# Performance work log

Measured on AMD Instinct MI355X. Metric: run time of the kernel, lower is better.

The kernel has to match this reference:

```python
import jax, jax.numpy as jnp
import numpy as np
from jax import lax

P = 8; E = 192; D_MODEL = E + 4; D_STATE = 16; D_CONV = 4; EXPAND = 2
D_INNER = EXPAND * D_MODEL  # 392
DT_RANK = -(-D_MODEL // 16)  # 13
MAX_FREQ = 32


def silu(v):
    return v * jax.nn.sigmoid(v)


def layernorm(v, g, b, eps=1e-5):
    m = v.mean(-1, keepdims=True)
    var = v.var(-1, keepdims=True)
    return (v - m) / jnp.sqrt(var + eps) * g + b


def mamba(x, in_w, conv_w, conv_b, xp_w, dt_w, dt_b, A_log, Dp, out_w):
    # Standard mamba_ssm Mamba block. x: (B, L, d_model)
    B, L, _ = x.shape
    xz = x @ in_w.T                      # (B,L,2*d_inner)
    xi, z = jnp.split(xz, 2, axis=-1)
    # depthwise causal conv1d (torch pads d_conv-1 both sides then truncates to L)
    xc = jnp.transpose(xi, (0, 2, 1))    # (B,d_inner,L)
    xc = lax.conv_general_dilated(xc, conv_w[:, None, :], (1,), [(D_CONV - 1, 0)],
                                  dimension_numbers=('NCH', 'OIH', 'NCH'),
                                  feature_group_count=D_INNER)
    xc = silu(jnp.transpose(xc, (0, 2, 1)) + conv_b)  # (B,L,d_inner)
    x_dbl = xc @ xp_w.T                  # (B,L,dt_rank+2*d_state)
    dt = x_dbl[..., :DT_RANK]
    Bm = x_dbl[..., DT_RANK:DT_RANK + D_STATE]
    Cm = x_dbl[..., DT_RANK + D_STATE:]
    delta = jax.nn.softplus(dt @ dt_w.T + dt_b)       # (B,L,d_inner)
    A = -jnp.exp(A_log)                               # (d_inner,d_state)
    deltaA = jnp.exp(delta[..., None] * A)            # (B,L,d_inner,d_state)
    deltaBu = delta[..., None] * Bm[:, :, None, :] * xc[..., None]

    def step(h, inp):
        dA, dBu, c = inp
        h = dA * h + dBu
        return h, jnp.einsum('bdn,bn->bd', h, c)

    h0 = jnp.zeros((B, D_INNER, D_STATE), x.dtype)
    _, ys = lax.scan(step, h0, (deltaA.transpose(1, 0, 2, 3),
                                deltaBu.transpose(1, 0, 2, 3),
                                Cm.transpose(1, 0, 2)))
    y = ys.transpose(1, 0, 2) + Dp * xc
    y = y * silu(z)
    return y @ out_w.T


def _mk_mamba_params(key):
    ks = jax.random.split(key, 6)
    s = 0.05
    return dict(
        in_w=jax.random.normal(ks[0], (2 * D_INNER, D_MODEL)) * s,
        conv_w=jax.random.normal(ks[1], (D_INNER, D_CONV)) * s,
        conv_b=jnp.zeros((D_INNER,)),
        xp_w=jax.random.normal(ks[2], (DT_RANK + 2 * D_STATE, D_INNER)) * s,
        dt_w=jax.random.normal(ks[3], (D_INNER, DT_RANK)) * s,
        dt_b=jax.random.normal(ks[4], (D_INNER,)) * 0.1,
        A_log=jnp.log(jnp.broadcast_to(jnp.arange(1, D_STATE + 1, dtype=jnp.float32), (D_INNER, D_STATE)) + 0.0),
        D=jnp.ones((D_INNER,)),
        out_w=jax.random.normal(ks[5], (D_MODEL, D_INNER)) * s,
    )


def setup_inputs() -> dict:
    key = jax.random.key(0)
    k = jax.random.split(key, 8)
    inp = {
        'x': jax.random.normal(k[0], (16, 3, 256, 256), dtype=jnp.float32),
        'patch_w': jax.random.normal(k[1], (E, 3, P, P)) * 0.05,
        'patch_b': jnp.zeros((E,)),
        'pe_ln_g': jnp.ones((E,)), 'pe_ln_b': jnp.zeros((E,)),
        'blk_ln_g': jnp.ones((D_MODEL,)), 'blk_ln_b': jnp.zeros((D_MODEL,)),
        'cls_w': jax.random.normal(k[2], (1, D_MODEL)) * 0.05,
        'cls_b': jnp.zeros((1,)),
    }
    for pref, kk in (('f_', k[3]), ('b_', k[4])):
        for name, val in _mk_mamba_params(kk).items():
            inp[pref + name] = val
    return inp


def reference(x, patch_w, patch_b, pe_ln_g, pe_ln_b,
              f_in_w, f_conv_w, f_conv_b, f_xp_w, f_dt_w, f_dt_b, f_A_log, f_D, f_out_w,
              b_in_w, b_conv_w, b_conv_b, b_xp_w, b_dt_w, b_dt_b, b_A_log, b_D, b_out_w,
              blk_ln_g, blk_ln_b, cls_w, cls_b):
    B, C, H, W = x.shape
    hp, wp = H // P, W // P
    # PatchEmbed: stride==kernel conv expressed as one GEMM over patches
    xp = x.reshape(B, C, hp, P, wp, P)
    tok = jnp.einsum('bchpwq,ecpq->bhwe', xp, patch_w) + patch_b
    tok = tok.reshape(B, hp * wp, E)
    tok = silu(layernorm(tok, pe_ln_g, pe_ln_b))
    # RotaryEmbedding: concat 4 positional channels
    L = hp * wp
    scale = 2 * np.pi / MAX_FREQ
    pos = jnp.arange(L, dtype=tok.dtype)[:, None] * scale
    row = (jnp.arange(L) // MAX_FREQ).astype(tok.dtype)[:, None] * scale
    cp = jnp.concatenate([jnp.sin(pos), jnp.cos(pos), jnp.sin(row), jnp.cos(row)], axis=-1)
    h = jnp.concatenate([tok, jnp.broadcast_to(cp[None], (B, L, 4))], axis=-1)  # (B,L,196)
    # BidirectionalMambaBlock
    fo = mamba(h, f_in_w, f_conv_w, f_conv_b, f_xp_w, f_dt_w, f_dt_b, f_A_log, f_D, f_out_w)
    bo = jnp.flip(mamba(jnp.flip(h, 1), b_in_w, b_conv_w, b_conv_b, b_xp_w, b_dt_w, b_dt_b, b_A_log, b_D, b_out_w), 1)
    out = (fo + bo) * 0.5
    out = silu(layernorm(out, blk_ln_g, blk_ln_b)) + h
    # Classifier: mean pool + linear (num_classes==2 -> 1 logit)
    return out.mean(1) @ cls_w.T + cls_b
```

## Files before the change

kernel.cpp:

```cpp
#include <hip/hip_runtime.h>
#include <cstdint>
#include <cstddef>

constexpr int B_   = 16;
constexpr int L_   = 1024;
constexpr int E_   = 192;
constexpr int DM   = 196;
constexpr int DI   = 392;
constexpr int DS   = 16;
constexpr int DTR  = 13;
constexpr int NTOK = B_ * L_;
constexpr int XDW  = DTR + 2 * DS;
constexpr int CH   = B_ * DI;

constexpr int KP_XZ = 224;
constexpr int KP_OP = 416;
constexpr int KP_PW = 192;

constexpr size_t HW_SZ = (size_t)NTOK * DM;
constexpr size_t DI_SZ = (size_t)NTOK * DI;

constexpr size_t O_H     = 0;
constexpr size_t O_H16   = 3211264;
constexpr size_t O_XI_F  = 5046272;
constexpr size_t O_XI_B  = 11468800;
constexpr size_t O_Z_F   = 17891328;
constexpr size_t O_Z_B   = 24313856;
constexpr size_t O_XC_F  = 30736384;
constexpr size_t O_XC_B  = 37158912;
constexpr size_t O_DTR_F = 43581440;
constexpr size_t O_DTR_B = 43794432;
constexpr size_t O_BC_F  = 44007424;
constexpr size_t O_BC_B  = 44531712;
constexpr size_t O_YS_F  = 45056000;
constexpr size_t O_YS_B  = 48267264;
constexpr size_t O_PW16  = 51478528;
constexpr size_t O_FIN16 = 51496960;
constexpr size_t O_BIN16 = 51584768;
constexpr size_t O_FOUT16= 51672576;
constexpr size_t O_BOUT16= 51713344;

typedef _Float16 half8 __attribute__((ext_vector_type(8)));
typedef _Float16 half4v __attribute__((ext_vector_type(4)));
typedef float f32x4v __attribute__((ext_vector_type(4)));

__device__ __forceinline__ float siluf(float x) {
    return x / (1.f + __expf(-x));
}
__device__ __forceinline__ float fexp2(float x) {
    return __builtin_amdgcn_exp2f(x);
}

__device__ __forceinline__ float blk_sum(float v, float* red) {
    #pragma unroll
    for (int o = 32; o > 0; o >>= 1) v += __shfl_down(v, o);
    int w = threadIdx.x >> 6;
    __syncthreads();
    if ((threadIdx.x & 63) == 0) red[w] = v;
    __syncthreads();
    return red[0] + red[1] + red[2] + red[3];
}

__global__ __launch_bounds__(256) void cvt_all(const float* __restrict__ pw,
                                               const float* __restrict__ fin,
                                               const float* __restrict__ bin,
                                               const float* __restrict__ fout,
                                               const float* __restrict__ bout,
                                               _Float16* __restrict__ dst) {
    int i = blockIdx.x * 256 + threadIdx.x;
    const float* src; int K, Kp, off;
    if (i < 36864)       { src = pw;   K = 192; Kp = 192; off = i; }
    else if (i < 212480) { src = fin;  K = 196; Kp = 224; off = i - 36864; }
    else if (i < 388096) { src = bin;  K = 196; Kp = 224; off = i - 212480; }
    else if (i < 469632) { src = fout; K = 392; Kp = 416; off = i - 388096; }
    else                 { src = bout; K = 392; Kp = 416; off = i - 469632; }
    int n = off / Kp, k = off - n * Kp;
    dst[i] = (_Float16)(k < K ? src[(size_t)n * K + k] : 0.f);
}

__global__ __launch_bounds__(256) void gather_patch(const float* __restrict__ x,
                                                    _Float16* __restrict__ Xp) {
    int i = blockIdx.x * 256 + threadIdx.x;
    int tok = i / 24, r = i - tok * 24;
    int c = r >> 3, p = r & 7;
    int b = tok >> 10, l = tok & 1023, hh = l >> 5, wv = l & 31;
    const float* src = x + (((size_t)(b * 3 + c) * 256 + hh * 8 + p) << 8) + wv * 8;
    float4 v0 = *(const float4*)src;
    float4 v1 = *(const float4*)(src + 4);
    half8 o;
    o[0] = (_Float16)v0.x; o[1] = (_Float16)v0.y; o[2] = (_Float16)v0.z; o[3] = (_Float16)v0.w;
    o[4] = (_Float16)v1.x; o[5] = (_Float16)v1.y; o[6] = (_Float16)v1.z; o[7] = (_Float16)v1.w;
    *(half8*)(Xp + (size_t)tok * 192 + c * 64 + p * 8) = o;
}

template <int MODE>
__device__ __forceinline__ void mfma_core(const _Float16* __restrict__ A,
                                          const _Float16* __restrict__ W,
                                          const float* __restrict__ bias,
                                          void* __restrict__ Cv_,
                                          int N, int Kpad, int ldc,
                                          int flip, int m_blk, int n_blk) {
    const int tid = threadIdx.x;
    const int wv = tid >> 6, lane = tid & 63;
    const int col = lane & 15, quad = lane >> 4;
    const int m_base = m_blk * 128 + wv * 32;
    const int n_base = n_blk * 64;

    int r0 = m_base + col, r1 = m_base + 16 + col;
    if (flip) {
        r0 = (r0 & ~1023) + (1023 - (r0 & 1023));
        r1 = (r1 & ~1023) + (1023 - (r1 & 1023));
    }
    const _Float16* a0p = A + (size_t)r0 * Kpad + quad * 8;
    const _Float16* a1p = A + (size_t)r1 * Kpad + quad * 8;

    const _Float16* bp[4];
    bool bok[4];
    #pragma unroll
    for (int j = 0; j < 4; ++j) {
        int n = n_base + j * 16 + col;
        bok[j] = (n < N);
        bp[j] = W + (size_t)(bok[j] ? n : 0) * Kpad + quad * 8;
    }

    f32x4v acc[2][4];
    #pragma unroll
    for (int i = 0; i < 2; ++i)
        #pragma unroll
        for (int j = 0; j < 4; ++j)
            #pragma unroll
            for (int r = 0; r < 4; ++r) acc[i][j][r] = 0.f;

    half8 bzero;
    #pragma unroll
    for (int q = 0; q < 8; ++q) bzero[q] = (_Float16)0.f;

    for (int k0 = 0; k0 < Kpad; k0 += 32) {
        half8 a0 = *(const half8*)(a0p + k0);
        half8 a1 = *(const half8*)(a1p + k0);
        #pragma unroll
        for (int j = 0; j < 4; ++j) {
            half8 bv = bzero;
            if (bok[j]) bv = *(const half8*)(bp[j] + k0);
            acc[0][j] = __builtin_amdgcn_mfma_f32_16x16x32_f16(a0, bv, acc[0][j], 0, 0, 0);
            acc[1][j] = __builtin_amdgcn_mfma_f32_16x16x32_f16(a1, bv, acc[1][j], 0, 0, 0);
        }
    }

    if constexpr (MODE == 0) {
        float* C = (float*)Cv_;
        #pragma unroll
        for (int i = 0; i < 2; ++i) {
            int mrow = m_base + i * 16 + quad * 4;
            #pragma unroll
            for (int j = 0; j < 4; ++j) {
                int n = n_base + j * 16 + col;
                if (n < N) {
                    float bv = bias ? bias[n] : 0.f;
                    #pragma unroll
                    for (int r = 0; r < 4; ++r)
                        C[(size_t)(mrow + r) * ldc + n] = acc[i][j][r] + bv;
                }
            }
        }
    } else if constexpr (MODE == 2 || MODE == 3) {
        __shared__ _Float16 cst[64 * 136];
        #pragma unroll
        for (int i = 0; i < 2; ++i) {
            int t_loc = wv * 32 + i * 16 + quad * 4;
            #pragma unroll
            for (int j = 0; j < 4; ++j) {
                int n_loc = j * 16 + col;
                half4v v;
                #pragma unroll
                for (int r = 0; r < 4; ++r) {
                    float xx = acc[i][j][r];
                    if (MODE == 3) xx = xx / (1.f + __expf(-xx));
                    v[r] = (_Float16)xx;
                }
                *(half4v*)&cst[n_loc * 136 + t_loc] = v;
            }
        }
        __syncthreads();
        const int n_loc = tid >> 2, chunk = tid & 3;
        const int n = n_base + n_loc;
        if (n < N) {
            const int bb = (m_blk * 128) >> 10;
            const int t0b = (m_blk * 128) & 1023;
            _Float16* dst = (_Float16*)Cv_ + (((size_t)(bb * N + n)) << 10) + t0b + chunk * 32;
            const _Float16* s = &cst[n_loc * 136 + chunk * 32];
            #pragma unroll
            for (int q = 0; q < 4; ++q)
                *(half8*)(dst + q * 8) = *(const half8*)(s + q * 8);
        }
    } else {
        __shared__ _Float16 cst[128 * 72];
        #pragma unroll
        for (int i = 0; i < 2; ++i) {
            #pragma unroll
            for (int j = 0; j < 4; ++j) {
                int n_loc = j * 16 + col;
                #pragma unroll
                for (int r = 0; r < 4; ++r) {
                    int m_loc = wv * 32 + i * 16 + quad * 4 + r;
                    cst[m_loc * 72 + n_loc] = (_Float16)acc[i][j][r];
                }
            }
        }
        __syncthreads();
        const int m_loc = tid >> 1, half = tid & 1;
        const int m = m_blk * 128 + m_loc;
        _Float16* C = (_Float16*)Cv_;
        const _Float16* s = &cst[m_loc * 72 + half * 32];
        if (n_base + 64 <= N) {
            _Float16* dst = C + (size_t)m * ldc + n_base + half * 32;
            #pragma unroll
            for (int q = 0; q < 4; ++q)
                *(half8*)(dst + q * 8) = *(const half8*)(s + q * 8);
        } else {
            #pragma unroll
            for (int q = 0; q < 32; ++q) {
                int n = n_base + half * 32 + q;
                if (n < N) C[(size_t)m * ldc + n] = s[q];
            }
        }
    }
}

__global__ __launch_bounds__(256) void mfma_patch(const _Float16* __restrict__ A,
                                                  const _Float16* __restrict__ W,
                                                  const float* __restrict__ bias,
                                                  float* __restrict__ C) {
    mfma_core<0>(A, W, bias, C, 192, KP_PW, 192, 0, blockIdx.x, blockIdx.y);
}

__global__ __launch_bounds__(256) void mfma_xz(const _Float16* __restrict__ A,
                                               const _Float16* __restrict__ Wf,
                                               const _Float16* __restrict__ Wb,
                                               _Float16* __restrict__ C0, _Float16* __restrict__ C1,
                                               _Float16* __restrict__ C2, _Float16* __restrict__ C3) {
    const int zi = blockIdx.z;
    const _Float16* W = (zi < 2 ? Wf : Wb) + (size_t)(zi & 1) * DI * KP_XZ;
    const int flip = zi >> 1;
    if (zi == 0)      mfma_core<2>(A, W, nullptr, C0, DI, KP_XZ, 0, flip, blockIdx.x, blockIdx.y);
    else if (zi == 1) mfma_core<3>(A, W, nullptr, C1, DI, KP_XZ, 0, flip, blockIdx.x, blockIdx.y);
    else if (zi == 2) mfma_core<2>(A, W, nullptr, C2, DI, KP_XZ, 0, flip, blockIdx.x, blockIdx.y);
    else              mfma_core<3>(A, W, nullptr, C3, DI, KP_XZ, 0, flip, blockIdx.x, blockIdx.y);
}

__global__ __launch_bounds__(256) void mfma_op(const _Float16* __restrict__ Af,
                                               const _Float16* __restrict__ Ab,
                                               const _Float16* __restrict__ Wf,
                                               const _Float16* __restrict__ Wb,
                                               _Float16* __restrict__ Cf, _Float16* __restrict__ Cb) {
    const int zi = blockIdx.z;
    mfma_core<4>(zi ? Ab : Af, zi ? Wb : Wf, nullptr, zi ? Cb : Cf,
                 DM, KP_OP, DM, 0, blockIdx.x, blockIdx.y);
}

__global__ __launch_bounds__(256) void ln_silu_pos(const float* __restrict__ tok,
                                                   const float* __restrict__ g,
                                                   const float* __restrict__ bb,
                                                   _Float16* __restrict__ h16) {
    const int w = threadIdx.x >> 6, lane = threadIdx.x & 63;
    const int t = blockIdx.x * 4 + w;
    const float* tp = tok + (size_t)t * E_;
    float v[3];
    float s1 = 0.f, s2 = 0.f;
    #pragma unroll
    for (int i = 0; i < 3; ++i) {
        v[i] = tp[lane + i * 64];
        s1 += v[i];
        s2 = fmaf(v[i], v[i], s2);
    }
    #pragma unroll
    for (int o = 32; o > 0; o >>= 1) {
        s1 += __shfl_xor(s1, o);
        s2 += __shfl_xor(s2, o);
    }
    float mean = s1 * (1.f / E_);
    float var = s2 * (1.f / E_) - mean * mean;
    float inv = rsqrtf(var + 1e-5f);
    _Float16* hq = h16 + (size_t)t * KP_XZ;
    #pragma unroll
    for (int i = 0; i < 3; ++i) {
        int e = lane + i * 64;
        float o = siluf((v[i] - mean) * inv * g[e] + bb[e]);
        hq[e] = (_Float16)o;
    }
    const int l = t & 1023;
    const float scale = 0.19634954084936207f;
    if (lane < 4) {
        float pv = (lane == 0) ? sinf(l * scale)
                 : (lane == 1) ? cosf(l * scale)
                 : (lane == 2) ? sinf((float)(l >> 5) * scale)
                 :               cosf((float)(l >> 5) * scale);
        hq[E_ + lane] = (_Float16)pv;
    } else if (lane < 32) {
        hq[192 + lane] = (_Float16)0.f;
    }
}

__global__ __launch_bounds__(256) void gemm_xdbl(const _Float16* __restrict__ xi_f,
                                                 const _Float16* __restrict__ xi_b,
                                                 const float* __restrict__ Wf,
                                                 const float* __restrict__ Wb,
                                                 const float* __restrict__ fcw,
                                                 const float* __restrict__ fcb,
                                                 const float* __restrict__ bcw,
                                                 const float* __restrict__ bcb,
                                                 float* __restrict__ dtrf,
                                                 float* __restrict__ dtrb,
                                                 float* __restrict__ bcf,
                                                 float* __restrict__ bcb2,
                                                 _Float16* __restrict__ xcf,
                                                 _Float16* __restrict__ xcb) {
    const int yi = blockIdx.y;
    const _Float16* xi = yi ? xi_b : xi_f;
    const float* W = yi ? Wb : Wf;
    const float* cw = yi ? bcw : fcw;
    const float* cb = yi ? bcb : fcb;
    float* dtr = yi ? dtrb : dtrf;
    float* bc = yi ? bcb2 : bcf;
    _Float16* xc = yi ? xcb : xcf;
    __shared__ __align__(16) float As[16][68];
    __shared__ __align__(16) float Ws[16][68];
    const int m0 = blockIdx.x * 64;
    const int t = threadIdx.x;
    const int tx = t & 15, ty = t >> 4;
    float acc[4][4] = {};
    const int arow_l = t >> 2;
    const int kq = (t & 3) * 4;
    const int bb_ = m0 >> 10, tt0 = m0 & 1023;
    for (int kt = 0; kt < 25; ++kt) {
        const int k0 = kt << 4;
        {
            int kr = t >> 4, tc = t & 15;
            int kk = k0 + kr;
            float o4[4] = {0.f, 0.f, 0.f, 0.f};
            if (kk < DI) {
                const int tpos = tt0 + tc * 4;
                const _Float16* xp = xi + (((size_t)(bb_ * DI + kk)) << 10) + tpos;
                half4v cur = *(const half4v*)xp;
                half4v prv;
                if (tpos > 0) prv = *(const half4v*)(xp - 4);
                else { prv[0] = prv[1] = prv[2] = prv[3] = (_Float16)0.f; }
                float xw[7] = {(float)prv[1], (float)prv[2], (float)prv[3],
                               (float)cur[0], (float)cur[1], (float)cur[2], (float)cur[3]};
                float4 wv4 = *(const float4*)(cw + kk * 4);
                float wc[4] = {wv4.x, wv4.y, wv4.z, wv4.w};
                float bv = cb[kk];
                #pragma unroll
                for (int j = 0; j < 4; ++j) {
                    float a = bv;
                    #pragma unroll
                    for (int q = 0; q < 4; ++q) a = fmaf(xw[j + q], wc[q], a);
                    o4[j] = siluf(a);
                }
                half4v o4h;
                #pragma unroll
                for (int j = 0; j < 4; ++j) o4h[j] = (_Float16)o4[j];
                *(half4v*)(xc + (((size_t)(bb_ * DI + kk)) << 10) + tpos) = o4h;
            }
            *(float4*)&As[kr][tc * 4] = *(float4*)o4;
        }
        {
            bool okn = arow_l < XDW;
            const float* wp = W + (size_t)arow_l * DI;
            #pragma unroll
            for (int jj = 0; jj < 4; ++jj) {
                int kk = k0 + kq + jj;
                Ws[kq + jj][arow_l] = (okn && kk < DI) ? wp[kk] : 0.f;
            }
        }
        __syncthreads();
        #pragma unroll
        for (int k = 0; k < 16; ++k) {
            float av[4], wv[4];
            *(float4*)av = *(const float4*)&As[k][ty * 4];
            *(float4*)wv = *(const float4*)&Ws[k][tx * 4];
            #pragma unroll
            for (int i = 0; i < 4; ++i)
                #pragma unroll
                for (int j = 0; j < 4; ++j)
                    acc[i][j] = fmaf(av[i], wv[j], acc[i][j]);
        }
        __syncthreads();
    }
    #pragma unroll
    for (int i = 0; i < 4; ++i) {
        int m = m0 + ty * 4 + i;
        #pragma unroll
        for (int j = 0; j < 4; ++j) {
            int n = tx * 4 + j;
            float v = acc[i][j];
            if (n < DTR) dtr[(size_t)m * DTR + n] = v;
            else if (n < XDW) bc[(size_t)m * 32 + (n - DTR)] = v;
        }
    }
}

__global__ __launch_bounds__(256) void delta_kernel(
        const float* __restrict__ dtr_f, const float* __restrict__ dtr_b,
        _Float16* __restrict__ dlT_f, _Float16* __restrict__ dlT_b,
        const float* __restrict__ f_dt_w, const float* __restrict__ f_dt_b,
        const float* __restrict__ b_dt_w, const float* __restrict__ b_dt_b) {
    int i = blockIdx.x * 256 + threadIdx.x;
    int dir = i >= (int)DI_SZ;
    int j = dir ? i - (int)DI_SZ : i;
    int r = j >> 10, t = j & 1023;
    int b = r / DI, d = r - (r / DI) * DI;
    size_t tok = ((size_t)b << 10) + t;
    const float* xd = (dir ? dtr_b : dtr_f) + tok * DTR;
    const float* w = (dir ? b_dt_w : f_dt_w) + d * DTR;
    float acc = (dir ? b_dt_b : f_dt_b)[d];
    #pragma unroll
    for (int q = 0; q < DTR; ++q) acc = fmaf(xd[q], w[q], acc);
    float sp = fmaxf(acc, 0.f) + log1pf(__expf(-fabsf(acc)));
    (dir ? dlT_b : dlT_f)[j] = (_Float16)sp;
}

__global__ __launch_bounds__(256) __attribute__((amdgpu_waves_per_eu(4, 4)))
void scan_kernel(
        const _Float16* __restrict__ dlT_f, const _Float16* __restrict__ dlT_b,
        const _Float16* __restrict__ xcT_f, const _Float16* __restrict__ xcT_b,
        const float* __restrict__ bc_f,  const float* __restrict__ bc_b,
        const _Float16* __restrict__ zT_f, const _Float16* __restrict__ zT_b,
        _Float16* __restrict__ y16_f,    _Float16* __restrict__ y16_b,
        const float* __restrict__ fA, const float* __restrict__ bA,
        const float* __restrict__ fD, const float* __restrict__ bD) {
    __shared__ float sH[256][17];
    __shared__ float sPI[256][17];
    const int tid = threadIdx.x;
    const int ch_l = tid & 7;
    const int c    = tid >> 3;
    const int row  = tid;
    const int blk  = (blockIdx.x & 7) * 196 + (blockIdx.x >> 3);
    const int chain = blk * 8 + ch_l;
    const int dir = chain >= CH;
    const int r = chain - (dir ? CH : 0);
    const int b = r / DI, d = r - (r / DI) * DI;

    const _Float16* dlT = (dir ? dlT_b : dlT_f) + ((size_t)r << 10);
    const _Float16* uT  = (dir ? xcT_b : xcT_f) + ((size_t)r << 10);
    const _Float16* zT  = (dir ? zT_b : zT_f) + ((size_t)r << 10);
    const float* BC  = (dir ? bc_b  : bc_f)  + (((size_t)b << 10) * 32);
    _Float16* y16    = (dir ? y16_b : y16_f) + ((size_t)r << 10);
    const float* Al  = (dir ? bA : fA) + d * DS;
    float Av[16];
    #pragma unroll
    for (int i = 0; i < 16; ++i) Av[i] = -__expf(Al[i]) * 1.4426950408889634f;
    const float Dd = (dir ? bD : fD)[d];
    const int t0 = c << 5;

    if (c < 31) {
        float h[16];
        #pragma unroll
        for (int i = 0; i < 16; ++i) h[i] = 0.f;
        float S = 0.f;
        const float* bcp = BC + t0 * 32;
        const _Float16* dp = dlT + t0;
        const _Float16* up = uT + t0;
        for (int g = 0; g < 8; ++g) {
            half4v d4 = *(const half4v*)(dp + g * 4);
            half4v u4 = *(const half4v*)(up + g * 4);
            #pragma unroll
            for (int tt = 0; tt < 4; ++tt) {
                float dv = (float)d4[tt];
                float uv = (float)u4[tt];
                float w = dv * uv;
                S += dv;
                #pragma unroll
                for (int q = 0; q < 4; ++q) {
                    float4 Bq = *(const float4*)(bcp + tt * 32 + q * 4);
                    h[q*4+0] = fmaf(fexp2(dv * Av[q*4+0]), h[q*4+0], w * Bq.x);
                    h[q*4+1] = fmaf(fexp2(dv * Av[q*4+1]), h[q*4+1], w * Bq.y);
                    h[q*4+2] = fmaf(fexp2(dv * Av[q*4+2]), h[q*4+2], w * Bq.z);
                    h[q*4+3] = fmaf(fexp2(dv * Av[q*4+3]), h[q*4+3], w * Bq.w);
                }
            }
            bcp += 128;
        }
        #pragma unroll
        for (int i = 0; i < 16; ++i) {
            sPI[row][i] = fexp2(S * Av[i]);
            sH[row][i] = h[i];
        }
    }
    __syncthreads();

    if (tid < 128) {
        const int ch = tid >> 4, n = tid & 15;
        float hi = 0.f;
        #pragma unroll
        for (int cc = 0; cc < 32; ++cc) {
            const int rw = (cc << 3) | ch;
            float P = sPI[rw][n];
            float H = sH[rw][n];
            sPI[rw][n] = hi;
            if (cc < 31) hi = fmaf(P, hi, H);
        }
    }
    __syncthreads();

    {
        float h[16];
        #pragma unroll
        for (int i = 0; i < 16; ++i) h[i] = sPI[row][i];
        const float* bcp = BC + t0 * 32;
        const _Float16* dp = dlT + t0;
        const _Float16* up = uT + t0;
        const _Float16* zp = zT + t0;
        _Float16* yp = y16 + t0;
        for (int g8 = 0; g8 < 4; ++g8) {
            half8 zb = *(const half8*)(zp + g8 * 8);
            _Float16 ybuf[8] __attribute__((aligned(16)));
            #pragma unroll
            for (int gg = 0; gg < 2; ++gg) {
                half4v d4 = *(const half4v*)(dp + g8 * 8 + gg * 4);
                half4v u4 = *(const half4v*)(up + g8 * 8 + gg * 4);
                #pragma unroll
                for (int tt = 0; tt < 4; ++tt) {
                    float dv = (float)d4[tt];
                    float uv = (float)u4[tt];
                    float w = dv * uv;
                    float p = 0.f;
                    #pragma unroll
                    for (int q = 0; q < 4; ++q) {
                        float4 Bq = *(const float4*)(bcp + tt * 32 + q * 4);
                        float4 Cq = *(const float4*)(bcp + tt * 32 + 16 + q * 4);
                        h[q*4+0] = fmaf(fexp2(dv * Av[q*4+0]), h[q*4+0], w * Bq.x);
                        p = fmaf(h[q*4+0], Cq.x, p);
                        h[q*4+1] = fmaf(fexp2(dv * Av[q*4+1]), h[q*4+1], w * Bq.y);
                        p = fmaf(h[q*4+1], Cq.y, p);
                        h[q*4+2] = fmaf(fexp2(dv * Av[q*4+2]), h[q*4+2], w * Bq.z);
                        p = fmaf(h[q*4+2], Cq.z, p);
                        h[q*4+3] = fmaf(fexp2(dv * Av[q*4+3]), h[q*4+3], w * Bq.w);
                        p = fmaf(h[q*4+3], Cq.w, p);
                    }
                    ybuf[gg * 4 + tt] =
                        (_Float16)((p + Dd * uv) * (float)zb[gg * 4 + tt]);
                }
                bcp += 128;
            }
            *(half8*)(yp + g8 * 8) = *(half8*)ybuf;
        }
    }
}

__global__ __launch_bounds__(256) void transp_y(
        const _Float16* __restrict__ yf, const _Float16* __restrict__ yb,
        _Float16* __restrict__ of, _Float16* __restrict__ ob) {
    __shared__ _Float16 tile[64][72];
    const int dblk = blockIdx.z % 7, dir = blockIdx.z / 7;
    const int b = blockIdx.y, tb = blockIdx.x;
    const _Float16* y = dir ? yb : yf;
    _Float16* o = dir ? ob : of;
    const int d0 = dblk * 64, t0 = tb * 64;
    const int dl = threadIdx.x >> 2, ts = (threadIdx.x & 3) * 16;
    const int d = d0 + dl;
    if (d < DI) {
        const _Float16* src = y + (((size_t)(b * DI + d)) << 10) + t0 + ts;
        *(half8*)&tile[dl][ts] = *(const half8*)src;
        *(half8*)&tile[dl][ts + 8] = *(const half8*)(src + 8);
    } else {
        #pragma unroll
        for (int q = 0; q < 16; ++q) tile[dl][ts + q] = (_Float16)0.f;
    }
    __syncthreads();
    const int tl = threadIdx.x >> 2, ds = (threadIdx.x & 3) * 16;
    if (d0 + ds < KP_OP) {
        _Float16 v[16] __attribute__((aligned(16)));
        #pragma unroll
        for (int q = 0; q < 16; ++q) v[q] = tile[ds + q][tl];
        _Float16* dst = o + ((size_t)((b << 10) + t0 + tl)) * KP_OP + d0 + ds;
        *(half8*)dst = *(half8*)&v[0];
        *(half8*)(dst + 8) = *(half8*)&v[8];
    }
}

__global__ __launch_bounds__(256) void final_head(
        const _Float16* __restrict__ fo, const _Float16* __restrict__ bo,
        const _Float16* __restrict__ h16, const float* __restrict__ g,
        const float* __restrict__ bb, const float* __restrict__ cls_w,
        float* __restrict__ partial) {
    const int w = threadIdx.x >> 6, lane = threadIdx.x & 63;
    const int t = blockIdx.x * 4 + w;
    const int b = t >> 10, l = t & 1023;
    const _Float16* fp = fo + (size_t)t * DM;
    const _Float16* bp = bo + ((size_t)(b << 10) + (1023 - l)) * DM;
    const _Float16* hp = h16 + (size_t)t * KP_XZ;
    float v[4];
    float s1 = 0.f, s2 = 0.f;
    #pragma unroll
    for (int i = 0; i < 4; ++i) {
        int e = lane + i * 64;
        bool ok = (i < 3) || (lane < 4);
        float vv = ok ? 0.5f * ((float)fp[e] + (float)bp[e]) : 0.f;
        v[i] = vv;
        s1 += vv;
        s2 = fmaf(vv, vv, s2);
    }
    #pragma unroll
    for (int o = 32; o > 0; o >>= 1) {
        s1 += __shfl_xor(s1, o);
        s2 += __shfl_xor(s2, o);
    }
    float mean = s1 * (1.f / DM);
    float var = s2 * (1.f / DM) - mean * mean;
    float inv = rsqrtf(var + 1e-5f);
    float c = 0.f;
    #pragma unroll
    for (int i = 0; i < 4; ++i) {
        int e = lane + i * 64;
        bool ok = (i < 3) || (lane < 4);
        if (ok) {
            float o2 = (v[i] - mean) * inv * g[e] + bb[e];
            o2 = siluf(o2) + (float)hp[e];
            c = fmaf(o2, cls_w[e], c);
        }
    }
    #pragma unroll
    for (int o = 32; o > 0; o >>= 1) c += __shfl_xor(c, o);
    if (lane == 0) partial[t] = c;
}

__global__ __launch_bounds__(256) void head_reduce(const float* __restrict__ partial,
                                                   const float* __restrict__ cls_b,
                                                   float* __restrict__ out) {
    __shared__ float red[4];
    const int b = blockIdx.x;
    const float* p = partial + ((size_t)b << 10);
    float s = 0.f;
    for (int i = threadIdx.x; i < 1024; i += 256) s += p[i];
    s = blk_sum(s, red);
    if (threadIdx.x == 0) out[b] = s * (1.f / 1024.f) + cls_b[0];
}

extern "C" void kernel_launch(void* const* d_in, const int* in_sizes, int n_in,
                              void* d_out, int out_size, void* d_ws, size_t ws_size,
                              hipStream_t stream) {
    const float* x        = (const float*)d_in[0];
    const float* patch_w  = (const float*)d_in[1];
    const float* patch_b  = (const float*)d_in[2];
    const float* pe_g     = (const float*)d_in[3];
    const float* pe_b     = (const float*)d_in[4];
    const float* blk_g    = (const float*)d_in[5];
    const float* blk_b    = (const float*)d_in[6];
    const float* cls_w    = (const float*)d_in[7];
    const float* cls_b    = (const float*)d_in[8];
    const float* f_in_w   = (const float*)d_in[9];
    const float* f_conv_w = (const float*)d_in[10];
    const float* f_conv_b = (const float*)d_in[11];
    const float* f_xp_w   = (const float*)d_in[12];
    const float* f_dt_w   = (const float*)d_in[13];
    const float* f_dt_b   = (const float*)d_in[14];
    const float* f_A_log  = (const float*)d_in[15];
    const float* f_D      = (const float*)d_in[16];
    const float* f_out_w  = (const float*)d_in[17];
    const float* b_in_w   = (const float*)d_in[18];
    const float* b_conv_w = (const float*)d_in[19];
    const float* b_conv_b = (const float*)d_in[20];
    const float* b_xp_w   = (const float*)d_in[21];
    const float* b_dt_w   = (const float*)d_in[22];
    const float* b_dt_b   = (const float*)d_in[23];
    const float* b_A_log  = (const float*)d_in[24];
    const float* b_D      = (const float*)d_in[25];
    const float* b_out_w  = (const float*)d_in[26];

    float* ws = (float*)d_ws;
    float* out = (float*)d_out;

    _Float16* H16    = (_Float16*)(ws + O_H16);
    _Float16* XI16f  = (_Float16*)(ws + O_XI_F);
    _Float16* XI16b  = (_Float16*)(ws + O_XI_B);
    _Float16* DL16f  = (_Float16*)(ws + O_XI_F);
    _Float16* DL16b  = (_Float16*)(ws + O_XI_B);
    _Float16* FO16   = (_Float16*)(ws + O_XI_F);
    _Float16* BO16   = (_Float16*)(ws + O_XI_B);
    _Float16* ZT16f  = (_Float16*)(ws + O_Z_F);
    _Float16* ZT16b  = (_Float16*)(ws + O_Z_B);
    _Float16* YsTf16 = (_Float16*)(ws + O_Z_F);
    _Float16* YsTb16 = (_Float16*)(ws + O_Z_B);
    _Float16* XC16f  = (_Float16*)(ws + O_XC_F);
    _Float16* XC16b  = (_Float16*)(ws + O_XC_B);
    float* PART      = ws + O_XC_F;
    float* DTRf      = ws + O_DTR_F;
    float* DTRb      = ws + O_DTR_B;
    float* BCf       = ws + O_BC_F;
    float* BCb       = ws + O_BC_B;
    _Float16* Xp16   = (_Float16*)(ws + O_YS_F);
    float* TokRaw    = ws + O_YS_B;
    _Float16* Y16f   = (_Float16*)(ws + O_YS_F);
    _Float16* Y16b   = (_Float16*)(ws + O_YS_B);
    _Float16* PW16   = (_Float16*)(ws + O_PW16);
    _Float16* FIN16  = (_Float16*)(ws + O_FIN16);
    _Float16* BIN16  = (_Float16*)(ws + O_BIN16);
    _Float16* FOUT16 = (_Float16*)(ws + O_FOUT16);
    _Float16* BOUT16 = (_Float16*)(ws + O_BOUT16);

    cvt_all<<<2153, 256, 0, stream>>>(patch_w, f_in_w, b_in_w, f_out_w, b_out_w, PW16);

    gather_patch<<<(NTOK * 24) / 256, 256, 0, stream>>>(x, Xp16);
    mfma_patch<<<dim3(NTOK / 128, 3), 256, 0, stream>>>(Xp16, PW16, patch_b, TokRaw);
    ln_silu_pos<<<NTOK / 4, 256, 0, stream>>>(TokRaw, pe_g, pe_b, H16);

    mfma_xz<<<dim3(NTOK / 128, 7, 4), 256, 0, stream>>>(H16, FIN16, BIN16,
                                                        XI16f, ZT16f, XI16b, ZT16b);
    gemm_xdbl<<<dim3(NTOK / 64, 2), 256, 0, stream>>>(
        XI16f, XI16b, f_xp_w, b_xp_w, f_conv_w, f_conv_b, b_conv_w, b_conv_b,
        DTRf, DTRb, BCf, BCb, XC16f, XC16b);
    delta_kernel<<<(2 * (int)DI_SZ) / 256, 256, 0, stream>>>(
        DTRf, DTRb, DL16f, DL16b, f_dt_w, f_dt_b, b_dt_w, b_dt_b);
    scan_kernel<<<2 * CH / 8, 256, 0, stream>>>(
        DL16f, DL16b, XC16f, XC16b, BCf, BCb, ZT16f, ZT16b, Y16f, Y16b,
        f_A_log, b_A_log, f_D, b_D);
    transp_y<<<dim3(16, 16, 14), 256, 0, stream>>>(Y16f, Y16b, YsTf16, YsTb16);
    mfma_op<<<dim3(NTOK / 128, 4, 2), 256, 0, stream>>>(YsTf16, YsTb16,
                                                        FOUT16, BOUT16, FO16, BO16);
    final_head<<<NTOK / 4, 256, 0, stream>>>(FO16, BO16, H16, blk_g, blk_b, cls_w, PART);
    head_reduce<<<B_, 256, 0, stream>>>(PART, cls_b, out);
}
```

Measured before the change: 519.3 us.

## Split scan state across thread pairs and use longer time chunks

Restructures the chunked selective scan so each chain's 16 state dimensions are split across two lanes (8 each), and each thread handles a 64-step chunk instead of 32, giving 16 chunks per chain. Partial C·h dot products are combined with a lane shuffle, and each lane writes half of the outputs. This cuts per-thread register pressure and the serial cross-chunk combine length, but it duplicates the delta, u and z loads and the exp work across the lane pair. It also lengthens the serial per-chunk loop. Launch bounds change from fixed waves-per-EU to a minimum of 2 blocks.

```diff
diff --git a/kernel.cpp b/kernel.cpp
--- a/kernel.cpp
+++ b/kernel.cpp
@@ -420,8 +420,7 @@
     (dir ? dlT_b : dlT_f)[j] = (_Float16)sp;
 }
 
-__global__ __launch_bounds__(256) __attribute__((amdgpu_waves_per_eu(4, 4)))
-void scan_kernel(
+__global__ __launch_bounds__(256, 2) void scan_kernel(
         const _Float16* __restrict__ dlT_f, const _Float16* __restrict__ dlT_b,
         const _Float16* __restrict__ xcT_f, const _Float16* __restrict__ xcT_b,
         const float* __restrict__ bc_f,  const float* __restrict__ bc_b,
@@ -429,12 +428,12 @@
         _Float16* __restrict__ y16_f,    _Float16* __restrict__ y16_b,
         const float* __restrict__ fA, const float* __restrict__ bA,
         const float* __restrict__ fD, const float* __restrict__ bD) {
-    __shared__ float sH[256][17];
-    __shared__ float sPI[256][17];
+    __shared__ float sH[8][16][17];
+    __shared__ float sPI[8][16][17];
     const int tid = threadIdx.x;
-    const int ch_l = tid & 7;
-    const int c    = tid >> 3;
-    const int row  = tid;
+    const int ni   = tid & 1;
+    const int c    = (tid >> 1) & 15;
+    const int ch_l = tid >> 5;
     const int blk  = (blockIdx.x & 7) * 196 + (blockIdx.x >> 3);
     const int chain = blk * 8 + ch_l;
     const int dir = chain >= CH;
@@ -444,24 +443,22 @@
     const _Float16* dlT = (dir ? dlT_b : dlT_f) + ((size_t)r << 10);
     const _Float16* uT  = (dir ? xcT_b : xcT_f) + ((size_t)r << 10);
     const _Float16* zT  = (dir ? zT_b : zT_f) + ((size_t)r << 10);
-    const float* BC  = (dir ? bc_b  : bc_f)  + (((size_t)b << 10) * 32);
+    const float* BC  = (dir ? bc_b  : bc_f)  + (((size_t)b << 10) * 32) + ni * 8;
     _Float16* y16    = (dir ? y16_b : y16_f) + ((size_t)r << 10);
-    const float* Al  = (dir ? bA : fA) + d * DS;
-    float Av[16];
-    #pragma unroll
-    for (int i = 0; i < 16; ++i) Av[i] = -__expf(Al[i]) * 1.4426950408889634f;
+    const float* Al  = (dir ? bA : fA) + d * DS + ni * 8;
+    float Av[8];
+    #pragma unroll
+    for (int i = 0; i < 8; ++i) Av[i] = -__expf(Al[i]) * 1.4426950408889634f;
     const float Dd = (dir ? bD : fD)[d];
-    const int t0 = c << 5;
-
-    if (c < 31) {
-        float h[16];
-        #pragma unroll
-        for (int i = 0; i < 16; ++i) h[i] = 0.f;
+    const int t0 = c << 6;
+
+    if (c < 15) {
+        float h[8] = {0.f, 0.f, 0.f, 0.f, 0.f, 0.f, 0.f, 0.f};
         float S = 0.f;
-        const float* bcp = BC + t0 * 32;
+        const float* bcp = BC + (size_t)t0 * 32;
         const _Float16* dp = dlT + t0;
         const _Float16* up = uT + t0;
-        for (int g = 0; g < 8; ++g) {
+        for (int g = 0; g < 16; ++g) {
             half4v d4 = *(const half4v*)(dp + g * 4);
             half4v u4 = *(const half4v*)(up + g * 4);
             #pragma unroll
@@ -471,7 +468,7 @@
                 float w = dv * uv;
                 S += dv;
                 #pragma unroll
-                for (int q = 0; q < 4; ++q) {
+                for (int q = 0; q < 2; ++q) {
                     float4 Bq = *(const float4*)(bcp + tt * 32 + q * 4);
                     h[q*4+0] = fmaf(fexp2(dv * Av[q*4+0]), h[q*4+0], w * Bq.x);
                     h[q*4+1] = fmaf(fexp2(dv * Av[q*4+1]), h[q*4+1], w * Bq.y);
@@ -482,9 +479,9 @@
             bcp += 128;
         }
         #pragma unroll
-        for (int i = 0; i < 16; ++i) {
-            sPI[row][i] = fexp2(S * Av[i]);
-            sH[row][i] = h[i];
+        for (int i = 0; i < 8; ++i) {
+            sPI[ch_l][c][ni * 8 + i] = fexp2(S * Av[i]);
+            sH[ch_l][c][ni * 8 + i] = h[i];
         }
     }
     __syncthreads();
@@ -493,32 +490,32 @@
         const int ch = tid >> 4, n = tid & 15;
         float hi = 0.f;
         #pragma unroll
-        for (int cc = 0; cc < 32; ++cc) {
-            const int rw = (cc << 3) | ch;
-            float P = sPI[rw][n];
-            float H = sH[rw][n];
-            sPI[rw][n] = hi;
-            if (cc < 31) hi = fmaf(P, hi, H);
+        for (int cc = 0; cc < 16; ++cc) {
+            float P = sPI[ch][cc][n];
+            float H = sH[ch][cc][n];
+            sPI[ch][cc][n] = hi;
+            if (cc < 15) hi = fmaf(P, hi, H);
         }
     }
     __syncthreads();
 
     {
-        float h[16];
-        #pragma unroll
-        for (int i = 0; i < 16; ++i) h[i] = sPI[row][i];
-        const float* bcp = BC + t0 * 32;
+        float h[8];
+        #pragma unroll
+        for (int i = 0; i < 8; ++i) h[i] = sPI[ch_l][c][ni * 8 + i];
+        const float* bcp = BC + (size_t)t0 * 32;
         const _Float16* dp = dlT + t0;
         const _Float16* up = uT + t0;
         const _Float16* zp = zT + t0;
         _Float16* yp = y16 + t0;
-        for (int g8 = 0; g8 < 4; ++g8) {
-            half8 zb = *(const half8*)(zp + g8 * 8);
-            _Float16 ybuf[8] __attribute__((aligned(16)));
-            #pragma unroll
-            for (int gg = 0; gg < 2; ++gg) {
-                half4v d4 = *(const half4v*)(dp + g8 * 8 + gg * 4);
-                half4v u4 = *(const half4v*)(up + g8 * 8 + gg * 4);
+        for (int w8 = 0; w8 < 2; ++w8) {
+            _Float16 ybuf[16] __attribute__((aligned(16)));
+            #pragma unroll
+            for (int gg = 0; gg < 8; ++gg) {
+                const int tb = w8 * 32 + gg * 4;
+                half4v d4 = *(const half4v*)(dp + tb);
+                half4v u4 = *(const half4v*)(up + tb);
+                half4v z4 = *(const half4v*)(zp + tb);
                 #pragma unroll
                 for (int tt = 0; tt < 4; ++tt) {
                     float dv = (float)d4[tt];
@@ -526,7 +523,7 @@
                     float w = dv * uv;
                     float p = 0.f;
                     #pragma unroll
-                    for (int q = 0; q < 4; ++q) {
+                    for (int q = 0; q < 2; ++q) {
                         float4 Bq = *(const float4*)(bcp + tt * 32 + q * 4);
                         float4 Cq = *(const float4*)(bcp + tt * 32 + 16 + q * 4);
                         h[q*4+0] = fmaf(fexp2(dv * Av[q*4+0]), h[q*4+0], w * Bq.x);
@@ -538,12 +535,16 @@
                         h[q*4+3] = fmaf(fexp2(dv * Av[q*4+3]), h[q*4+3], w * Bq.w);
                         p = fmaf(h[q*4+3], Cq.w, p);
                     }
-                    ybuf[gg * 4 + tt] =
-                        (_Float16)((p + Dd * uv) * (float)zb[gg * 4 + tt]);
+                    p += __shfl_xor(p, 1);
+                    if ((gg >> 2) == ni)
+                        ybuf[(gg & 3) * 4 + tt] =
+                            (_Float16)((p + Dd * uv) * (float)z4[tt]);
                 }
                 bcp += 128;
             }
-            *(half8*)(yp + g8 * 8) = *(half8*)ybuf;
+            _Float16* dst = yp + w8 * 32 + ni * 16;
+            *(half8*)dst = *(half8*)&ybuf[0];
+            *(half8*)(dst + 8) = *(half8*)&ybuf[8];
         }
     }
 }
```

After: 544.2 us. 1.05x slower.
